# Optimization experiments

Hardware: AMD Instinct MI355X
Metric: run time of the kernel (lower is better)

The kernel has to match this reference:

```python
import jax, jax.numpy as jnp
import numpy as np

B, S, D_IN, D_OUT, R = 4, 1024, 1024, 1024, 8

def setup_inputs() -> dict:
    key = jax.random.key(0)
    k1, k2, k3, k4, k5 = jax.random.split(key, 5)
    scale = 1.0 / np.sqrt(D_IN)
    return {
        "x": jax.random.normal(k1, (B, S, D_IN), dtype=jnp.float32),
        "A_params": jax.random.normal(k2, (B, S, D_OUT, R), dtype=jnp.float32) * 0.02,
        "B_params": jax.random.normal(k3, (B, S, R, D_IN), dtype=jnp.float32) * 0.02,
        "W": jax.random.normal(k4, (D_OUT, D_IN), dtype=jnp.float32) * scale,
        "b": jax.random.normal(k5, (D_OUT,), dtype=jnp.float32) * scale,
    }

def reference(x, A_params, B_params, W, b):
    # base linear: y = x @ W^T + b  -> [B, S, D_OUT]
    base_out = jnp.einsum('bsi,oi->bso', x, W) + b
    # per-token low-rank update: (x @ B^T) @ A^T
    inter = jnp.einsum('bsi,bsri->bsr', x, B_params)           # [B, S, R]
    adaptation = jnp.einsum('bsr,bsor->bso', inter, A_params)  # [B, S, D_OUT]
    return base_out + adaptation
```

## Files before the change

### kernel.cpp

```cpp
#include <hip/hip_runtime.h>
#include <hip/hip_bf16.h>
#include <stdint.h>

#define TOKENS 4096
#define DIN 1024
#define DOUT 1024
#define RANK 8

typedef __attribute__((ext_vector_type(4))) float f32x4;
typedef __attribute__((ext_vector_type(8))) short short8;

__device__ __forceinline__ unsigned short f2bf(float f) {
    union { float f; unsigned u; } v; v.f = f;
    unsigned r = v.u + 0x7FFFu + ((v.u >> 16) & 1u);
    return (unsigned short)(r >> 16);
}

__global__ __launch_bounds__(256) void k_convert_w(const float* __restrict__ W,
                                                   ushort* __restrict__ Wb) {
    int i = blockIdx.x * 256 + threadIdx.x;
    float4 v = ((const float4*)W)[i];
    ushort4 u;
    u.x = f2bf(v.x); u.y = f2bf(v.y); u.z = f2bf(v.z); u.w = f2bf(v.w);
    ((ushort4*)Wb)[i] = u;
}

__global__ __launch_bounds__(256) void k_inter(const float* __restrict__ x,
                                               const float* __restrict__ Bp,
                                               float* __restrict__ inter,
                                               ushort* __restrict__ xb) {
    const int t = blockIdx.x;
    const int tid = threadIdx.x;
    const int lane = tid & 63, wave = tid >> 6;

    float4 xv = ((const float4*)(x + (size_t)t * DIN))[tid];

    ushort4 u;
    u.x = f2bf(xv.x); u.y = f2bf(xv.y); u.z = f2bf(xv.z); u.w = f2bf(xv.w);
    ((ushort4*)(xb + (size_t)t * DIN))[tid] = u;

    const float4* B4 = (const float4*)(Bp + (size_t)t * RANK * DIN);
    float acc[RANK];
#pragma unroll
    for (int r = 0; r < RANK; ++r) {
        float4 bv = B4[r * 256 + tid];
        acc[r] = xv.x * bv.x + xv.y * bv.y + xv.z * bv.z + xv.w * bv.w;
    }

    __shared__ float part[4][RANK];
#pragma unroll
    for (int r = 0; r < RANK; ++r) {
        float v = acc[r];
#pragma unroll
        for (int off = 32; off > 0; off >>= 1) v += __shfl_xor(v, off, 64);
        if (lane == 0) part[wave][r] = v;
    }
    __syncthreads();
    if (tid < RANK)
        inter[(size_t)t * RANK + tid] =
            part[0][tid] + part[1][tid] + part[2][tid] + part[3][tid];
}

__global__ __launch_bounds__(256) void k_gemm_fused(const ushort* __restrict__ Xb,
                                                    const ushort* __restrict__ Wb,
                                                    const float* __restrict__ bias,
                                                    const float* __restrict__ inter,
                                                    const float* __restrict__ Ap,
                                                    float* __restrict__ out) {
    __shared__ ushort As[128 * 64];
    __shared__ ushort Bs[64 * 64];
    __shared__ float sInter[128 * 9];
    __shared__ float sBias[64];

    const int tid = threadIdx.x;
    const int lane = tid & 63, wave = tid >> 6;
    const int wm = wave >> 1, wn = wave & 1;
    const int M0 = blockIdx.y * 128;
    const int N0 = blockIdx.x * 64;
    const int col16 = lane & 15;
    const int kg = lane >> 4;

    {
        float4 v = ((const float4*)(inter + (size_t)M0 * RANK))[tid];
        float* p = sInter + (tid >> 1) * 9 + (tid & 1) * 4;
        p[0] = v.x; p[1] = v.y; p[2] = v.z; p[3] = v.w;
        if (tid < 16) ((float4*)sBias)[tid] = ((const float4*)(bias + N0))[tid];
    }

    f32x4 acc[4][2] = {};

    for (int kt = 0; kt < DIN; kt += 64) {
        __syncthreads();
#pragma unroll
        for (int it = 0; it < 4; ++it) {
            int flat = it * 256 + tid;
            int row = flat >> 3, ch = flat & 7;
            const ushort* g = Xb + (size_t)(M0 + row) * DIN + kt + ch * 8;
            __builtin_amdgcn_global_load_lds(
                (const __attribute__((address_space(1))) void*)g,
                (__attribute__((address_space(3))) void*)(As + flat * 8), 16, 0, 0);
        }
#pragma unroll
        for (int it = 0; it < 2; ++it) {
            int flat = it * 256 + tid;
            int row = flat >> 3, ch = flat & 7;
            const ushort* g = Wb + (size_t)(N0 + row) * DIN + kt + ch * 8;
            __builtin_amdgcn_global_load_lds(
                (const __attribute__((address_space(1))) void*)g,
                (__attribute__((address_space(3))) void*)(Bs + flat * 8), 16, 0, 0);
        }
        asm volatile("s_waitcnt vmcnt(0)" ::: "memory");
        __syncthreads();

#pragma unroll
        for (int ks = 0; ks < 2; ++ks) {
            short8 a[4], b[2];
#pragma unroll
            for (int mf = 0; mf < 4; ++mf)
                a[mf] = *(const short8*)(As + (wm * 64 + mf * 16 + col16) * 64 + ks * 32 + kg * 8);
#pragma unroll
            for (int nf = 0; nf < 2; ++nf)
                b[nf] = *(const short8*)(Bs + (wn * 32 + nf * 16 + col16) * 64 + ks * 32 + kg * 8);
#pragma unroll
            for (int mf = 0; mf < 4; ++mf)
#pragma unroll
                for (int nf = 0; nf < 2; ++nf)
                    acc[mf][nf] = __builtin_amdgcn_mfma_f32_16x16x32_bf16(
                        a[mf], b[nf], acc[mf][nf], 0, 0, 0);
        }
    }

#pragma unroll
    for (int nf = 0; nf < 2; ++nf) {
        const int oc = wn * 32 + nf * 16 + col16;
        const int o = N0 + oc;
        const float bb = sBias[oc];
#pragma unroll
        for (int mf = 0; mf < 4; ++mf) {
#pragma unroll
            for (int rg = 0; rg < 4; ++rg) {
                const int mloc = wm * 64 + mf * 16 + kg * 4 + rg;
                const int m = M0 + mloc;
                const float4* A8 = (const float4*)(Ap + ((size_t)m * DOUT + o) * RANK);
                float4 a0 = A8[0], a1 = A8[1];
                const float* iv = sInter + mloc * 9;
                float ad = a0.x * iv[0] + a0.y * iv[1] + a0.z * iv[2] + a0.w * iv[3] +
                           a1.x * iv[4] + a1.y * iv[5] + a1.z * iv[6] + a1.w * iv[7];
                out[(size_t)m * DOUT + o] = acc[mf][nf][rg] + bb + ad;
            }
        }
    }
}

extern "C" void kernel_launch(void* const* d_in, const int* in_sizes, int n_in,
                              void* d_out, int out_size, void* d_ws, size_t ws_size,
                              hipStream_t stream) {
    const float* x    = (const float*)d_in[0];
    const float* Ap   = (const float*)d_in[1];
    const float* Bp   = (const float*)d_in[2];
    const float* W    = (const float*)d_in[3];
    const float* bias = (const float*)d_in[4];
    float* out = (float*)d_out;

    ushort* xb = (ushort*)d_ws;
    ushort* Wb = xb + (size_t)TOKENS * DIN;
    float* inter = (float*)(Wb + (size_t)DOUT * DIN);

    hipLaunchKernelGGL(k_convert_w, dim3(DOUT * DIN / 1024), dim3(256), 0, stream, W, Wb);
    hipLaunchKernelGGL(k_inter, dim3(TOKENS), dim3(256), 0, stream, x, Bp, inter, xb);
    hipLaunchKernelGGL(k_gemm_fused, dim3(DOUT / 64, TOKENS / 128), dim3(256), 0, stream,
                       xb, Wb, bias, inter, Ap, out);
}
```

Before: 82.25 us.

## Overlap per-token A_params loads and adaptation dot products with GEMM k-loop

The large A_params tensor (128 MiB) was previously read entirely in the epilogue after the GEMM finished. The change spreads those loads across the 16 k-iterations, two output elements per iteration, issued alongside the global-to-LDS tile loads. The rank-8 dot products are computed after each MFMA step and parked in a 32 KiB shared buffer that the epilogue then reads. This hides A_params memory traffic behind the MFMA work, but the larger LDS footprint may lower occupancy, and the vmcnt(0) wait now also blocks on the A loads.

```diff
diff --git a/kernel.cpp b/kernel.cpp
--- a/kernel.cpp
+++ b/kernel.cpp
@@ -69,8 +69,9 @@
                                                     float* __restrict__ out) {
     __shared__ ushort As[128 * 64];
     __shared__ ushort Bs[64 * 64];
-    __shared__ float sInter[128 * 9];
+    __shared__ float sInter[128 * 8];
     __shared__ float sBias[64];
+    __shared__ float sums[32 * 256];
 
     const int tid = threadIdx.x;
     const int lane = tid & 63, wave = tid >> 6;
@@ -80,20 +81,20 @@
     const int col16 = lane & 15;
     const int kg = lane >> 4;
 
-    {
-        float4 v = ((const float4*)(inter + (size_t)M0 * RANK))[tid];
-        float* p = sInter + (tid >> 1) * 9 + (tid & 1) * 4;
-        p[0] = v.x; p[1] = v.y; p[2] = v.z; p[3] = v.w;
-        if (tid < 16) ((float4*)sBias)[tid] = ((const float4*)(bias + N0))[tid];
-    }
+    ((float4*)sInter)[tid] = ((const float4*)(inter + (size_t)M0 * RANK))[tid];
+    if (tid < 16) ((float4*)sBias)[tid] = ((const float4*)(bias + N0))[tid];
+
+    const float* Abase = Ap + ((size_t)(M0 + wm * 64 + kg * 4) * DOUT +
+                               (N0 + wn * 32 + col16)) * RANK;
 
     f32x4 acc[4][2] = {};
 
-    for (int kt = 0; kt < DIN; kt += 64) {
+    for (int it = 0; it < 16; ++it) {
+        const int kt = it * 64;
         __syncthreads();
 #pragma unroll
-        for (int it = 0; it < 4; ++it) {
-            int flat = it * 256 + tid;
+        for (int st = 0; st < 4; ++st) {
+            int flat = st * 256 + tid;
             int row = flat >> 3, ch = flat & 7;
             const ushort* g = Xb + (size_t)(M0 + row) * DIN + kt + ch * 8;
             __builtin_amdgcn_global_load_lds(
@@ -101,14 +102,23 @@
                 (__attribute__((address_space(3))) void*)(As + flat * 8), 16, 0, 0);
         }
 #pragma unroll
-        for (int it = 0; it < 2; ++it) {
-            int flat = it * 256 + tid;
+        for (int st = 0; st < 2; ++st) {
+            int flat = st * 256 + tid;
             int row = flat >> 3, ch = flat & 7;
             const ushort* g = Wb + (size_t)(N0 + row) * DIN + kt + ch * 8;
             __builtin_amdgcn_global_load_lds(
                 (const __attribute__((address_space(1))) void*)g,
                 (__attribute__((address_space(3))) void*)(Bs + flat * 8), 16, 0, 0);
         }
+
+        const int nf = it >> 3, mf = (it >> 1) & 3, rg0 = (it & 1) * 2;
+        const float* Ae0 = Abase + ((size_t)(mf * 16 + rg0) * DOUT + nf * 16) * RANK;
+        const float* Ae1 = Ae0 + (size_t)DOUT * RANK;
+        float4 a00 = ((const float4*)Ae0)[0];
+        float4 a01 = ((const float4*)Ae0)[1];
+        float4 a10 = ((const float4*)Ae1)[0];
+        float4 a11 = ((const float4*)Ae1)[1];
+
         asm volatile("s_waitcnt vmcnt(0)" ::: "memory");
         __syncthreads();
 
@@ -116,18 +126,29 @@
         for (int ks = 0; ks < 2; ++ks) {
             short8 a[4], b[2];
 #pragma unroll
-            for (int mf = 0; mf < 4; ++mf)
-                a[mf] = *(const short8*)(As + (wm * 64 + mf * 16 + col16) * 64 + ks * 32 + kg * 8);
+            for (int m4 = 0; m4 < 4; ++m4)
+                a[m4] = *(const short8*)(As + (wm * 64 + m4 * 16 + col16) * 64 + ks * 32 + kg * 8);
 #pragma unroll
-            for (int nf = 0; nf < 2; ++nf)
-                b[nf] = *(const short8*)(Bs + (wn * 32 + nf * 16 + col16) * 64 + ks * 32 + kg * 8);
+            for (int n2 = 0; n2 < 2; ++n2)
+                b[n2] = *(const short8*)(Bs + (wn * 32 + n2 * 16 + col16) * 64 + ks * 32 + kg * 8);
 #pragma unroll
-            for (int mf = 0; mf < 4; ++mf)
+            for (int m4 = 0; m4 < 4; ++m4)
 #pragma unroll
-                for (int nf = 0; nf < 2; ++nf)
-                    acc[mf][nf] = __builtin_amdgcn_mfma_f32_16x16x32_bf16(
-                        a[mf], b[nf], acc[mf][nf], 0, 0, 0);
+                for (int n2 = 0; n2 < 2; ++n2)
+                    acc[m4][n2] = __builtin_amdgcn_mfma_f32_16x16x32_bf16(
+                        a[m4], b[n2], acc[m4][n2], 0, 0, 0);
         }
+
+        const int mloc0 = wm * 64 + mf * 16 + kg * 4 + rg0;
+        const float4* iv0 = (const float4*)(sInter + mloc0 * 8);
+        const float4* iv1 = (const float4*)(sInter + (mloc0 + 1) * 8);
+        float4 i00 = iv0[0], i01 = iv0[1], i10 = iv1[0], i11 = iv1[1];
+        float d0 = a00.x * i00.x + a00.y * i00.y + a00.z * i00.z + a00.w * i00.w +
+                   a01.x * i01.x + a01.y * i01.y + a01.z * i01.z + a01.w * i01.w;
+        float d1 = a10.x * i10.x + a10.y * i10.y + a10.z * i10.z + a10.w * i10.w +
+                   a11.x * i11.x + a11.y * i11.y + a11.z * i11.z + a11.w * i11.w;
+        sums[(it * 2) * 256 + tid] = d0;
+        sums[(it * 2 + 1) * 256 + tid] = d1;
     }
 
 #pragma unroll
@@ -139,14 +160,9 @@
         for (int mf = 0; mf < 4; ++mf) {
 #pragma unroll
             for (int rg = 0; rg < 4; ++rg) {
-                const int mloc = wm * 64 + mf * 16 + kg * 4 + rg;
-                const int m = M0 + mloc;
-                const float4* A8 = (const float4*)(Ap + ((size_t)m * DOUT + o) * RANK);
-                float4 a0 = A8[0], a1 = A8[1];
-                const float* iv = sInter + mloc * 9;
-                float ad = a0.x * iv[0] + a0.y * iv[1] + a0.z * iv[2] + a0.w * iv[3] +
-                           a1.x * iv[4] + a1.y * iv[5] + a1.z * iv[6] + a1.w * iv[7];
-                out[(size_t)m * DOUT + o] = acc[mf][nf][rg] + bb + ad;
+                const int m = M0 + wm * 64 + mf * 16 + kg * 4 + rg;
+                const int e = nf * 16 + mf * 4 + rg;
+                out[(size_t)m * DOUT + o] = acc[mf][nf][rg] + bb + sums[e * 256 + tid];
             }
         }
     }
```

New measurement: 73.41 us. 10.7% less time.
